# Optimization experiments

Hardware: AMD Instinct MI355X
Metric: run time of the kernel (lower is better)

Reference implementation:

```python
import jax, jax.numpy as jnp
import numpy as np

B, S, E, H = 2, 2048, 1024, 16
DH = E // H  # 64
EPS = 1e-5


def layer_norm(x, g, b):
    mu = jnp.mean(x, axis=-1, keepdims=True)
    var = jnp.mean(jnp.square(x - mu), axis=-1, keepdims=True)
    return (x - mu) * jax.lax.rsqrt(var + EPS) * g + b


def setup_inputs() -> dict:
    key = jax.random.key(0)
    ks = jax.random.split(key, 12)
    s = lambda fan_in: 1.0 / np.sqrt(fan_in)
    return {
        "x": jax.random.normal(ks[0], (B, S, E), dtype=jnp.float32),
        "ln1_g": jnp.ones((E,), jnp.float32),
        "ln1_b": jnp.zeros((E,), jnp.float32),
        # per-head projections, batched over head axis: [H, E, DH]
        "Wq": jax.random.uniform(ks[1], (H, E, DH), jnp.float32, -s(E), s(E)),
        "Wk": jax.random.uniform(ks[2], (H, E, DH), jnp.float32, -s(E), s(E)),
        "Wv": jax.random.uniform(ks[3], (H, E, DH), jnp.float32, -s(E), s(E)),
        "Wo": jax.random.uniform(ks[4], (H * DH, E), jnp.float32, -s(H * DH), s(H * DH)),
        "bo": jax.random.uniform(ks[5], (E,), jnp.float32, -s(H * DH), s(H * DH)),
        "ln2_g": jnp.ones((E,), jnp.float32),
        "ln2_b": jnp.zeros((E,), jnp.float32),
        "W1": jax.random.uniform(ks[6], (E, 4 * E), jnp.float32, -s(E), s(E)),
        "b1": jax.random.uniform(ks[7], (4 * E,), jnp.float32, -s(E), s(E)),
        "W2": jax.random.uniform(ks[8], (4 * E, E), jnp.float32, -s(4 * E), s(4 * E)),
        "b2": jax.random.uniform(ks[9], (E,), jnp.float32, -s(4 * E), s(4 * E)),
    }


def reference(x, ln1_g, ln1_b, Wq, Wk, Wv, Wo, bo, ln2_g, ln2_b, W1, b1, W2, b2):
    b, s, e = x.shape
    # --- multi-head attention (pre-LN) ---
    h = layer_norm(x, ln1_g, ln1_b)
    q = jnp.einsum("bse,hed->bhsd", h, Wq)
    k = jnp.einsum("bse,hed->bhsd", h, Wk)
    v = jnp.einsum("bse,hed->bhsd", h, Wv)
    # NOTE: original scales by channel**-0.5 (embed_size), not head_size
    scores = jnp.einsum("bhsd,bhtd->bhst", q, k) * (e ** -0.5)
    causal = jnp.tril(jnp.ones((s, s), dtype=bool))
    scores = jnp.where(causal, scores, -jnp.inf)
    attn = jax.nn.softmax(scores, axis=-1)  # dropout is identity in eval
    out = jnp.einsum("bhst,bhtd->bhsd", attn, v)
    out = out.transpose(0, 2, 1, 3).reshape(b, s, -1)  # concat heads: [B,S,H*DH]
    x = x + out @ Wo + bo
    # --- feed-forward (pre-LN) ---
    h2 = layer_norm(x, ln2_g, ln2_b)
    ff = jax.nn.relu(h2 @ W1 + b1) @ W2 + b2
    return x + ff
```

## Files before the change

kernel.cpp:

```cpp
#include <hip/hip_runtime.h>


typedef __bf16 bf16_t;
typedef __attribute__((ext_vector_type(8))) __bf16 bf16x8;
typedef __attribute__((ext_vector_type(4))) __bf16 bf16x4;
typedef __attribute__((ext_vector_type(4))) float f32x4;

#define B_DIM 2
#define S_DIM 2048
#define E_DIM 1024
#define H_DIM 16
#define DH_DIM 64

#define GLD16(gp, lp) __builtin_amdgcn_global_load_lds( \
    (const __attribute__((address_space(1))) void*)(gp), \
    (__attribute__((address_space(3))) void*)(lp), 16, 0, 0)

#define Q_SCALE 0.0450842120f

__global__ __launch_bounds__(256) void ln_kernel(
    const float* __restrict__ x, const float* __restrict__ g,
    const float* __restrict__ bv, bf16_t* __restrict__ out)
{
  const int row = blockIdx.x;
  const int t = threadIdx.x;
  const float* xr = x + (size_t)row * E_DIM;
  float4 v = *(const float4*)&xr[t * 4];
  float s  = v.x + v.y + v.z + v.w;
  float s2 = v.x*v.x + v.y*v.y + v.z*v.z + v.w*v.w;
#pragma unroll
  for (int m = 1; m < 64; m <<= 1) {
    s  += __shfl_xor(s,  m, 64);
    s2 += __shfl_xor(s2, m, 64);
  }
  __shared__ float red[8];
  const int wid = t >> 6, lane = t & 63;
  if (lane == 0) { red[wid] = s; red[4 + wid] = s2; }
  __syncthreads();
  s  = red[0] + red[1] + red[2] + red[3];
  s2 = red[4] + red[5] + red[6] + red[7];
  const float mu  = s * (1.f / E_DIM);
  const float var = s2 * (1.f / E_DIM) - mu * mu;
  const float rs  = rsqrtf(var + 1e-5f);
  float4 gg = *(const float4*)&g[t * 4];
  float4 bb = *(const float4*)&bv[t * 4];
  bf16x4 o;
  o[0] = (bf16_t)((v.x - mu) * rs * gg.x + bb.x);
  o[1] = (bf16_t)((v.y - mu) * rs * gg.y + bb.y);
  o[2] = (bf16_t)((v.z - mu) * rs * gg.z + bb.z);
  o[3] = (bf16_t)((v.w - mu) * rs * gg.w + bb.w);
  *(bf16x4*)&out[(size_t)row * E_DIM + t * 4] = o;
}

__global__ __launch_bounds__(256) void reduce2_ln(
    const float* __restrict__ p, const float* __restrict__ bo,
    const float* __restrict__ x, const float* __restrict__ g,
    const float* __restrict__ bv, float* __restrict__ xmid, bf16_t* __restrict__ h2)
{
  const int row = blockIdx.x;
  const int t = threadIdx.x;
  const size_t off = (size_t)row * E_DIM + t * 4;
  float4 a  = *(const float4*)&p[off];
  float4 b4 = *(const float4*)&p[(size_t)4096 * E_DIM + off];
  float4 xr = *(const float4*)&x[off];
  float4 bo4 = *(const float4*)&bo[t * 4];
  float4 v;
  v.x = a.x + b4.x + xr.x + bo4.x;
  v.y = a.y + b4.y + xr.y + bo4.y;
  v.z = a.z + b4.z + xr.z + bo4.z;
  v.w = a.w + b4.w + xr.w + bo4.w;
  *(float4*)&xmid[off] = v;
  float s  = v.x + v.y + v.z + v.w;
  float s2 = v.x*v.x + v.y*v.y + v.z*v.z + v.w*v.w;
#pragma unroll
  for (int m = 1; m < 64; m <<= 1) {
    s  += __shfl_xor(s,  m, 64);
    s2 += __shfl_xor(s2, m, 64);
  }
  __shared__ float red[8];
  const int wid = t >> 6, lane = t & 63;
  if (lane == 0) { red[wid] = s; red[4 + wid] = s2; }
  __syncthreads();
  s  = red[0] + red[1] + red[2] + red[3];
  s2 = red[4] + red[5] + red[6] + red[7];
  const float mu  = s * (1.f / E_DIM);
  const float var = s2 * (1.f / E_DIM) - mu * mu;
  const float rs  = rsqrtf(var + 1e-5f);
  float4 gg = *(const float4*)&g[t * 4];
  float4 bb = *(const float4*)&bv[t * 4];
  bf16x4 o;
  o[0] = (bf16_t)((v.x - mu) * rs * gg.x + bb.x);
  o[1] = (bf16_t)((v.y - mu) * rs * gg.y + bb.y);
  o[2] = (bf16_t)((v.z - mu) * rs * gg.z + bb.z);
  o[3] = (bf16_t)((v.w - mu) * rs * gg.w + bb.w);
  *(bf16x4*)&h2[off] = o;
}

__global__ __launch_bounds__(256) void reduce4(
    const bf16_t* __restrict__ p0, const bf16_t* __restrict__ p1,
    const bf16_t* __restrict__ p2, const bf16_t* __restrict__ p3,
    const float* __restrict__ b2, const float* __restrict__ xm,
    float* __restrict__ out)
{
  const int row = blockIdx.x;
  const int t = threadIdx.x;
  const size_t off = (size_t)row * E_DIM + t * 4;
  bf16x4 a0 = *(const bf16x4*)&p0[off];
  bf16x4 a1 = *(const bf16x4*)&p1[off];
  bf16x4 a2 = *(const bf16x4*)&p2[off];
  bf16x4 a3 = *(const bf16x4*)&p3[off];
  float4 xr = *(const float4*)&xm[off];
  float4 bb = *(const float4*)&b2[t * 4];
  float4 o;
  o.x = (float)a0[0] + (float)a1[0] + (float)a2[0] + (float)a3[0] + xr.x + bb.x;
  o.y = (float)a0[1] + (float)a1[1] + (float)a2[1] + (float)a3[1] + xr.y + bb.y;
  o.z = (float)a0[2] + (float)a1[2] + (float)a2[2] + (float)a3[2] + xr.z + bb.z;
  o.w = (float)a0[3] + (float)a1[3] + (float)a2[3] + (float)a3[3] + xr.w + bb.w;
  *(float4*)&out[off] = o;
}

__global__ __launch_bounds__(256) void transpose_cast(
    const float* __restrict__ src, bf16_t* __restrict__ dst, int R, int C)
{
  __shared__ float tile[64][65];
  const int c0 = blockIdx.x * 64, r0 = blockIdx.y * 64;
  const int t = threadIdx.x;
  const int rr = t >> 2;
#pragma unroll
  for (int u = 0; u < 4; u++) {
    const int cc = (t & 3) * 4 + u * 16;
    float4 f = *(const float4*)&src[(size_t)(r0 + rr) * C + c0 + cc];
    tile[rr][cc + 0] = f.x; tile[rr][cc + 1] = f.y;
    tile[rr][cc + 2] = f.z; tile[rr][cc + 3] = f.w;
  }
  __syncthreads();
  const int oc = t >> 2;
#pragma unroll
  for (int u = 0; u < 4; u++) {
    const int orr = (t & 3) * 4 + u * 16;
    bf16x4 w;
    w[0] = (bf16_t)tile[orr + 0][oc];
    w[1] = (bf16_t)tile[orr + 1][oc];
    w[2] = (bf16_t)tile[orr + 2][oc];
    w[3] = (bf16_t)tile[orr + 3][oc];
    *(bf16x4*)&dst[(size_t)(c0 + oc) * R + r0 + orr] = w;
  }
}

__global__ __launch_bounds__(256) void qkv_transpose(
    const float* __restrict__ Wq, const float* __restrict__ Wk,
    const float* __restrict__ Wv, bf16_t* __restrict__ dstT)
{
  const int m = blockIdx.y >> 4, h = blockIdx.y & 15;
  const float* src = (m == 0 ? Wq : (m == 1 ? Wk : Wv)) + (size_t)h * E_DIM * DH_DIM;
  const int e0 = blockIdx.x * 64;
  __shared__ float tile[64][65];
  const int t = threadIdx.x;
  const int rr = t >> 2;
#pragma unroll
  for (int u = 0; u < 4; u++) {
    const int cc = (t & 3) * 4 + u * 16;
    float4 f = *(const float4*)&src[(size_t)(e0 + rr) * DH_DIM + cc];
    tile[rr][cc + 0] = f.x; tile[rr][cc + 1] = f.y;
    tile[rr][cc + 2] = f.z; tile[rr][cc + 3] = f.w;
  }
  __syncthreads();
  const int oc = t >> 2;
  const size_t drow = (size_t)(m * 1024 + h * 64 + oc) * E_DIM;
#pragma unroll
  for (int u = 0; u < 4; u++) {
    const int orr = (t & 3) * 4 + u * 16;
    bf16x4 w;
    w[0] = (bf16_t)tile[orr + 0][oc];
    w[1] = (bf16_t)tile[orr + 1][oc];
    w[2] = (bf16_t)tile[orr + 2][oc];
    w[3] = (bf16_t)tile[orr + 3][oc];
    *(bf16x4*)&dstT[drow + e0 + orr] = w;
  }
}

constexpr int EPI_QKV = 0, EPI_BIAS_RELU = 2, EPI_PART_F32 = 3, EPI_PART_B16 = 4;

template <int EPI>
__global__ __launch_bounds__(256) void gemm_kernel(
    const bf16_t* __restrict__ A, const bf16_t* __restrict__ Bt,
    int M, int N, int Kst, int Klen,
    const float* __restrict__ bias, const float* __restrict__ resid,
    float* __restrict__ outF, bf16_t* __restrict__ outB,
    bf16_t* __restrict__ qo, bf16_t* __restrict__ ko, bf16_t* __restrict__ vo)
{
  __shared__ bf16_t As[2][128 * 32];
  __shared__ bf16_t Bs[2][128 * 32];
  const int gx = gridDim.x;
  const int nwg = gx * gridDim.y;
  int id = blockIdx.y * gx + blockIdx.x;
  id = (id & 7) * (nwg >> 3) + (id >> 3);
  const int m0 = (id % gx) * 128, n0 = (id / gx) * 128;
  const int sp = blockIdx.z;
  A  += (size_t)sp * Klen;
  Bt += (size_t)sp * Klen;

  const int tid = threadIdx.x, lane = tid & 63, wid = tid >> 6;
  const int wr = wid >> 1, wc = wid & 1;
  const int lr = lane & 15, lg = lane >> 4;
  const int rl = lane >> 2, k8 = (lane & 3) * 8;

  auto stage = [&](int buf, int k0) {
#pragma unroll
    for (int q = 0; q < 2; q++) {
      const int row = q * 64 + wid * 16 + rl;
      GLD16(A  + (size_t)(m0 + row) * Kst + k0 + k8, &As[buf][(q * 64 + wid * 16) * 32]);
      GLD16(Bt + (size_t)(n0 + row) * Kst + k0 + k8, &Bs[buf][(q * 64 + wid * 16) * 32]);
    }
  };

  const f32x4 z4 = {0.f, 0.f, 0.f, 0.f};
  f32x4 acc[4][4];
#pragma unroll
  for (int i = 0; i < 4; i++)
#pragma unroll
    for (int j = 0; j < 4; j++) acc[i][j] = z4;

  const int nt = Klen / 32;
  stage(0, 0);
  for (int it = 0; it < nt; ++it) {
    const int cur = it & 1;
    __syncthreads();
    if (it + 1 < nt) stage(cur ^ 1, (it + 1) * 32);
    bf16x8 af[4], bfr[4];
#pragma unroll
    for (int i = 0; i < 4; i++)
      af[i]  = *(const bf16x8*)&As[cur][(wr * 64 + i * 16 + lr) * 32 + lg * 8];
#pragma unroll
    for (int j = 0; j < 4; j++)
      bfr[j] = *(const bf16x8*)&Bs[cur][(wc * 64 + j * 16 + lr) * 32 + lg * 8];
    __builtin_amdgcn_s_setprio(1);
#pragma unroll
    for (int i = 0; i < 4; i++)
#pragma unroll
      for (int j = 0; j < 4; j++)
        acc[i][j] = __builtin_amdgcn_mfma_f32_16x16x32_bf16(af[i], bfr[j], acc[i][j], 0, 0, 0);
    __builtin_amdgcn_s_setprio(0);
  }

#pragma unroll
  for (int i = 0; i < 4; i++) {
#pragma unroll
    for (int j = 0; j < 4; j++) {
#pragma unroll
      for (int r = 0; r < 4; r++) {
        const int m = m0 + wr * 64 + i * 16 + lg * 4 + r;
        const int n = n0 + wc * 64 + j * 16 + lr;
        const float val = acc[i][j][r];
        if constexpr (EPI == EPI_QKV) {
          const int tsel = n >> 10, h = (n >> 6) & 15, d = n & 63;
          const int b = m >> 11, s = m & 2047;
          const size_t idx = ((size_t)((b * H_DIM + h) * S_DIM + s)) * DH_DIM + d;
          if (tsel == 0)      qo[idx] = (bf16_t)(val * Q_SCALE);
          else if (tsel == 1) ko[idx] = (bf16_t)val;
          else                vo[idx] = (bf16_t)val;
        } else if constexpr (EPI == EPI_BIAS_RELU) {
          const float u = val + bias[n];
          outB[(size_t)m * N + n] = (bf16_t)(u > 0.f ? u : 0.f);
        } else if constexpr (EPI == EPI_PART_F32) {
          outF[(size_t)sp * M * N + (size_t)m * N + n] = val;
        } else {
          bf16_t* o = sp == 0 ? outB : sp == 1 ? qo : sp == 2 ? ko : vo;
          o[(size_t)m * N + n] = (bf16_t)val;
        }
      }
    }
  }
}

__global__ __launch_bounds__(256) void attn_kernel(
    const bf16_t* __restrict__ Q, const bf16_t* __restrict__ K,
    const bf16_t* __restrict__ V, bf16_t* __restrict__ O,
    bf16_t* __restrict__ Opart, float* __restrict__ mpart, float* __restrict__ lpart)
{
  __shared__ bf16_t Ks[2][64 * 64];
  __shared__ bf16_t Vst[2][64 * 64];
  __shared__ bf16_t Ps[4][16 * 64];

  const int nwg = 80 * gridDim.y;
  int id = blockIdx.y * 80 + blockIdx.x;
  id = (id & 7) * (nwg >> 3) + (id >> 3);
  const int bx = id % 80, bh = id / 80;

  int qt, sp, ns;
  if (bx < 8)       { qt = bx;                sp = 0;            ns = 1; }
  else if (bx < 24) { qt = 8 + ((bx - 8) >> 1);  sp = (bx - 8) & 1;  ns = 2; }
  else if (bx < 48) { const int u = bx - 24; const int q3 = u / 3;
                      qt = 16 + q3;           sp = u - q3 * 3;   ns = 3; }
  else              { const int u = bx - 48;  qt = 24 + (u >> 2); sp = u & 3; ns = 4; }
  const int n = qt + 1;
  const int lo = (sp * n) / ns, hi = ((sp + 1) * n) / ns;

  const int q0b = qt * 64;
  const int tid = threadIdx.x;
  const int wid = tid >> 6, lane = tid & 63;
  const int lr = lane & 15, lg = lane >> 4;
  const int q0w = q0b + wid * 16;

  const bf16_t* Qp = Q + (size_t)bh * S_DIM * DH_DIM;
  const bf16_t* Kp = K + (size_t)bh * S_DIM * DH_DIM;
  const bf16_t* Vp = V + (size_t)bh * S_DIM * DH_DIM;

  bf16x8 bq[2];
#pragma unroll
  for (int c = 0; c < 2; c++)
    bq[c] = *(const bf16x8*)&Qp[(size_t)(q0w + lr) * DH_DIM + c * 32 + lg * 8];

  const f32x4 z4 = {0.f, 0.f, 0.f, 0.f};
  f32x4 Ot[4];
#pragma unroll
  for (int dt = 0; dt < 4; dt++) Ot[dt] = z4;
  float mrow = -1e30f, lrow = 0.f;

  const int st = tid >> 3;
  const int s8 = tid & 7;
  const int sbl = lane & 48;
  const int ktr = wid * 8 + (lane >> 3);
  const int ksc = (lane & 7);

  {
    const int t0 = lo * 64;
#pragma unroll
    for (int p = 0; p < 2; p++) {
      const int tr = p * 32 + ktr;
      GLD16(Kp + (size_t)(t0 + tr) * DH_DIM + (ksc ^ (tr & 7)) * 8,
            &Ks[0][(p * 32 + wid * 8) * 64]);
    }
  }
  bf16x8 vc0 = *(const bf16x8*)&Vp[(size_t)(lo * 64 + st) * DH_DIM + s8 * 8];
  bf16x8 vc1 = *(const bf16x8*)&Vp[(size_t)(lo * 64 + 32 + st) * DH_DIM + s8 * 8];
  bf16x8 vn0 = vc0, vn1 = vc1;

  for (int tc = lo; tc < hi; ++tc) {
    const int cur = (tc - lo) & 1;
#pragma unroll
    for (int h2 = 0; h2 < 2; h2++) {
      const bf16x8 vv = h2 ? vc1 : vc0;
      const int t = h2 * 32 + st;
#pragma unroll
      for (int j = 0; j < 8; j++) {
        const int d = s8 * 8 + j;
        const int f = j ^ s8;
        Vst[cur][(d * 128 + ((t * 2) ^ (f << 4))) >> 1] = vv[j];
      }
    }
    __syncthreads();
    if (tc + 1 < hi) {
      const int t1 = (tc + 1) * 64;
#pragma unroll
      for (int p = 0; p < 2; p++) {
        const int tr = p * 32 + ktr;
        GLD16(Kp + (size_t)(t1 + tr) * DH_DIM + (ksc ^ (tr & 7)) * 8,
              &Ks[cur ^ 1][(p * 32 + wid * 8) * 64]);
      }
      vn0 = *(const bf16x8*)&Vp[(size_t)(t1 + st) * DH_DIM + s8 * 8];
      vn1 = *(const bf16x8*)&Vp[(size_t)(t1 + 32 + st) * DH_DIM + s8 * 8];
    }

    const int t0 = tc * 64;
    f32x4 sc[4];
    __builtin_amdgcn_s_setprio(1);
#pragma unroll
    for (int j = 0; j < 4; j++) {
      f32x4 s = z4;
      const int t = j * 16 + lr;
#pragma unroll
      for (int c = 0; c < 2; c++) {
        const int kbyte = t * 128 + (((c * 4 + lg) * 16) ^ ((t & 7) << 4));
        bf16x8 ak = *(const bf16x8*)((const char*)&Ks[cur][0] + kbyte);
        s = __builtin_amdgcn_mfma_f32_16x16x32_bf16(ak, bq[c], s, 0, 0, 0);
      }
      sc[j] = s;
    }
    __builtin_amdgcn_s_setprio(0);
    if (tc == qt) {
#pragma unroll
      for (int j = 0; j < 4; j++)
#pragma unroll
        for (int r = 0; r < 4; r++) {
          const int tg = t0 + j * 16 + lg * 4 + r;
          if (tg > q0w + lr) sc[j][r] = -1e30f;
        }
    }
    float tmax = sc[0][0];
#pragma unroll
    for (int j = 0; j < 4; j++)
#pragma unroll
      for (int r = 0; r < 4; r++) tmax = fmaxf(tmax, sc[j][r]);
    tmax = fmaxf(tmax, __shfl_xor(tmax, 16, 64));
    tmax = fmaxf(tmax, __shfl_xor(tmax, 32, 64));
    const float mnew = fmaxf(mrow, tmax);
    const float fsc = __builtin_exp2f(mrow - mnew);
    mrow = mnew;
    float tsum = 0.f;
#pragma unroll
    for (int j = 0; j < 4; j++)
#pragma unroll
      for (int r = 0; r < 4; r++) {
        const float p = __builtin_exp2f(sc[j][r] - mnew);
        sc[j][r] = p;
        tsum += p;
      }
    tsum += __shfl_xor(tsum, 16, 64);
    tsum += __shfl_xor(tsum, 32, 64);
    lrow = lrow * fsc + tsum;

#pragma unroll
    for (int j = 0; j < 4; j++) {
      bf16x4 w;
#pragma unroll
      for (int r = 0; r < 4; r++) w[r] = (bf16_t)sc[j][r];
      const int pbyte = lr * 128 + ((j * 32 + lg * 8) ^ ((lr & 7) << 4));
      *(bf16x4*)((char*)&Ps[wid][0] + pbyte) = w;
    }
    float fr[4];
#pragma unroll
    for (int r = 0; r < 4; r++) fr[r] = __shfl(fsc, sbl | (lg * 4 + r), 64);
#pragma unroll
    for (int dt = 0; dt < 4; dt++)
#pragma unroll
      for (int r = 0; r < 4; r++) Ot[dt][r] *= fr[r];
    __builtin_amdgcn_s_setprio(1);
#pragma unroll
    for (int c = 0; c < 2; c++) {
      const int abyte = lr * 128 + ((c * 64 + lg * 16) ^ ((lr & 7) << 4));
      bf16x8 pa = *(const bf16x8*)((const char*)&Ps[wid][0] + abyte);
#pragma unroll
      for (int dt = 0; dt < 4; dt++) {
        const int d = dt * 16 + lr;
        const int f = (d & 7) ^ ((d >> 3) & 7);
        const int vbyte = d * 128 + (((c * 4 + lg) * 16) ^ (f << 4));
        bf16x8 bv = *(const bf16x8*)((const char*)&Vst[cur][0] + vbyte);
        Ot[dt] = __builtin_amdgcn_mfma_f32_16x16x32_bf16(pa, bv, Ot[dt], 0, 0, 0);
      }
    }
    __builtin_amdgcn_s_setprio(0);
    vc0 = vn0; vc1 = vn1;
  }

  if (ns == 1) {
    float linv[4];
#pragma unroll
    for (int r = 0; r < 4; r++)
      linv[r] = 1.f / __shfl(lrow, sbl | (lg * 4 + r), 64);
    const int b = bh >> 4, h = bh & 15;
#pragma unroll
    for (int r = 0; r < 4; r++) {
      const int s = q0w + lg * 4 + r;
      const size_t base = ((size_t)(b * S_DIM + s)) * E_DIM + h * DH_DIM;
#pragma unroll
      for (int dt = 0; dt < 4; dt++)
        O[base + dt * 16 + lr] = (bf16_t)(Ot[dt][r] * linv[r]);
    }
  } else {
    const int sbase = (qt < 16) ? 8 + 2 * (qt - 8)
                     : (qt < 24) ? 24 + 3 * (qt - 16) : 48 + 4 * (qt - 24);
    const int slot = bh * 80 + sbase + sp;
    bf16_t* Ob = Opart + (size_t)slot * 64 * 64;
#pragma unroll
    for (int r = 0; r < 4; r++)
#pragma unroll
      for (int dt = 0; dt < 4; dt++)
        Ob[(wid * 16 + lg * 4 + r) * 64 + dt * 16 + lr] = (bf16_t)Ot[dt][r];
    if (lg == 0) {
      mpart[slot * 64 + wid * 16 + lr] = mrow;
      lpart[slot * 64 + wid * 16 + lr] = lrow;
    }
  }
}

__global__ __launch_bounds__(256) void attn_combine(
    const bf16_t* __restrict__ Opart, const float* __restrict__ mpart,
    const float* __restrict__ lpart, bf16_t* __restrict__ O)
{
  const int qt = 8 + blockIdx.x;
  const int bh = blockIdx.y;
  const int ns = (qt < 16) ? 2 : (qt < 24) ? 3 : 4;
  const int sbase = (qt < 16) ? 8 + 2 * (qt - 8)
                   : (qt < 24) ? 24 + 3 * (qt - 16) : 48 + 4 * (qt - 24);
  const int slot0 = bh * 80 + sbase;
  const int tid = threadIdx.x;
  const int q = tid >> 2, d0 = (tid & 3) * 16;

  float M = -1e30f;
  for (int s = 0; s < ns; s++) M = fmaxf(M, mpart[(slot0 + s) * 64 + q]);
  float L = 0.f;
  float acc[16];
#pragma unroll
  for (int j = 0; j < 16; j++) acc[j] = 0.f;
  for (int s = 0; s < ns; s++) {
    const float w = __builtin_exp2f(mpart[(slot0 + s) * 64 + q] - M);
    L += w * lpart[(slot0 + s) * 64 + q];
    const bf16_t* Ob = Opart + ((size_t)(slot0 + s) * 64 + q) * 64 + d0;
    bf16x8 o0 = *(const bf16x8*)Ob;
    bf16x8 o1 = *(const bf16x8*)(Ob + 8);
#pragma unroll
    for (int j = 0; j < 8; j++) { acc[j] += w * (float)o0[j]; acc[8 + j] += w * (float)o1[j]; }
  }
  const float inv = 1.f / L;
  const int b = bh >> 4, h = bh & 15;
  const int srow = qt * 64 + q;
  bf16_t* out = O + ((size_t)(b * S_DIM + srow)) * E_DIM + h * DH_DIM + d0;
  bf16x8 w0, w1;
#pragma unroll
  for (int j = 0; j < 8; j++) { w0[j] = (bf16_t)(acc[j] * inv); w1[j] = (bf16_t)(acc[8 + j] * inv); }
  *(bf16x8*)out = w0;
  *(bf16x8*)(out + 8) = w1;
}

extern "C" void kernel_launch(void* const* d_in, const int* in_sizes, int n_in,
                              void* d_out, int out_size, void* d_ws, size_t ws_size,
                              hipStream_t stream)
{
  const float* x    = (const float*)d_in[0];
  const float* ln1g = (const float*)d_in[1];
  const float* ln1b = (const float*)d_in[2];
  const float* Wq   = (const float*)d_in[3];
  const float* Wk   = (const float*)d_in[4];
  const float* Wv   = (const float*)d_in[5];
  const float* Wo   = (const float*)d_in[6];
  const float* bo   = (const float*)d_in[7];
  const float* ln2g = (const float*)d_in[8];
  const float* ln2b = (const float*)d_in[9];
  const float* W1   = (const float*)d_in[10];
  const float* b1   = (const float*)d_in[11];
  const float* W2   = (const float*)d_in[12];
  const float* b2   = (const float*)d_in[13];

  char* ws = (char*)d_ws;
  bf16_t* WqkvT = (bf16_t*)(ws + 0);
  bf16_t* WoT   = (bf16_t*)(ws + 6291456);
  bf16_t* W1T   = (bf16_t*)(ws + 8388608);
  bf16_t* W2T   = (bf16_t*)(ws + 16777216);
  bf16_t* h1    = (bf16_t*)(ws + 25165824);
  bf16_t* qb    = (bf16_t*)(ws + 33554432);
  bf16_t* kb    = (bf16_t*)(ws + 41943040);
  bf16_t* vb    = (bf16_t*)(ws + 50331648);
  bf16_t* attnb = (bf16_t*)(ws + 58720256);
  float*  xmid  = (float* )(ws + 67108864);
  bf16_t* h2    = (bf16_t*)(ws + 83886080);
  bf16_t* ff1   = (bf16_t*)(ws + 25165824);
  bf16_t* Opart = (bf16_t*)(ws + 67108864);
  float*  mpart = (float* )(ws + 25165824);
  float*  lpart = (float* )(ws + 25821184);
  float*  po    = (float* )(ws + 25165824);
  bf16_t* pf0   = (bf16_t*)(ws + 0);
  bf16_t* pf1   = (bf16_t*)(ws + 8388608);
  bf16_t* pf2   = (bf16_t*)(ws + 58720256);
  bf16_t* pf3   = (bf16_t*)(ws + 83886080);

  qkv_transpose<<<dim3(16, 48), 256, 0, stream>>>(Wq, Wk, Wv, WqkvT);
  transpose_cast<<<dim3(16, 16), 256, 0, stream>>>(Wo, WoT, 1024, 1024);
  transpose_cast<<<dim3(64, 16), 256, 0, stream>>>(W1, W1T, 1024, 4096);
  transpose_cast<<<dim3(16, 64), 256, 0, stream>>>(W2, W2T, 4096, 1024);

  ln_kernel<<<4096, 256, 0, stream>>>(x, ln1g, ln1b, h1);
  gemm_kernel<EPI_QKV><<<dim3(32, 24, 1), 256, 0, stream>>>(
      h1, WqkvT, 4096, 3072, 1024, 1024, nullptr, nullptr,
      nullptr, nullptr, qb, kb, vb);
  attn_kernel<<<dim3(80, 32), 256, 0, stream>>>(qb, kb, vb, attnb, Opart, mpart, lpart);
  attn_combine<<<dim3(24, 32), 256, 0, stream>>>(Opart, mpart, lpart, attnb);
  gemm_kernel<EPI_PART_F32><<<dim3(32, 8, 2), 256, 0, stream>>>(
      attnb, WoT, 4096, 1024, 1024, 512, nullptr, nullptr,
      po, nullptr, nullptr, nullptr, nullptr);
  reduce2_ln<<<4096, 256, 0, stream>>>(po, bo, x, ln2g, ln2b, xmid, h2);
  gemm_kernel<EPI_BIAS_RELU><<<dim3(32, 32, 1), 256, 0, stream>>>(
      h2, W1T, 4096, 4096, 1024, 1024, b1, nullptr,
      nullptr, ff1, nullptr, nullptr, nullptr);
  gemm_kernel<EPI_PART_B16><<<dim3(32, 8, 4), 256, 0, stream>>>(
      ff1, W2T, 4096, 1024, 4096, 1024, nullptr, nullptr,
      nullptr, pf0, pf1, pf2, pf3);
  reduce4<<<4096, 256, 0, stream>>>(pf0, pf1, pf2, pf3, b2, xmid, (float*)d_out);

  (void)in_sizes; (void)n_in; (void)out_size; (void)ws_size;
}
```

Measured before the change: 284.9 us.

## Use 256x256 GEMM tiles with 512 threads, triple-buffered LDS and XOR swizzle

Replaces the 128x128, 256-thread GEMM with a 256x256 tile computed by 8 waves, each owning 128x64 of the output. LDS staging moves to a three-buffer ring with explicit vmcnt waits and raw barriers, so two tiles are in flight, and an XOR swizzle of the k-chunk is meant to reduce LDS bank conflicts. The aim is more data reuse per loaded byte and better latency hiding. The cost is fewer workgroups: the Wo GEMM gets only 128 blocks and the W2 GEMM 256, which can leave CUs idle on a 256-CU part. Register pressure also rises with 128 accumulator floats per thread.

```diff
diff --git a/kernel.cpp b/kernel.cpp
--- a/kernel.cpp
+++ b/kernel.cpp
@@ -182,80 +182,97 @@
 constexpr int EPI_QKV = 0, EPI_BIAS_RELU = 2, EPI_PART_F32 = 3, EPI_PART_B16 = 4;
 
 template <int EPI>
-__global__ __launch_bounds__(256) void gemm_kernel(
+__global__ __launch_bounds__(512, 2) void gemm256_kernel(
     const bf16_t* __restrict__ A, const bf16_t* __restrict__ Bt,
     int M, int N, int Kst, int Klen,
-    const float* __restrict__ bias, const float* __restrict__ resid,
+    const float* __restrict__ bias,
     float* __restrict__ outF, bf16_t* __restrict__ outB,
     bf16_t* __restrict__ qo, bf16_t* __restrict__ ko, bf16_t* __restrict__ vo)
 {
-  __shared__ bf16_t As[2][128 * 32];
-  __shared__ bf16_t Bs[2][128 * 32];
+  __shared__ bf16_t As[3][256 * 32];
+  __shared__ bf16_t Bs[3][256 * 32];
+
   const int gx = gridDim.x;
   const int nwg = gx * gridDim.y;
   int id = blockIdx.y * gx + blockIdx.x;
   id = (id & 7) * (nwg >> 3) + (id >> 3);
-  const int m0 = (id % gx) * 128, n0 = (id / gx) * 128;
+  const int m0 = (id % gx) * 256, n0 = (id / gx) * 256;
   const int sp = blockIdx.z;
   A  += (size_t)sp * Klen;
   Bt += (size_t)sp * Klen;
 
   const int tid = threadIdx.x, lane = tid & 63, wid = tid >> 6;
-  const int wr = wid >> 1, wc = wid & 1;
+  const int wm = wid >> 2, wn = wid & 3;
   const int lr = lane & 15, lg = lane >> 4;
-  const int rl = lane >> 2, k8 = (lane & 3) * 8;
-
-  auto stage = [&](int buf, int k0) {
-#pragma unroll
-    for (int q = 0; q < 2; q++) {
-      const int row = q * 64 + wid * 16 + rl;
-      GLD16(A  + (size_t)(m0 + row) * Kst + k0 + k8, &As[buf][(q * 64 + wid * 16) * 32]);
-      GLD16(Bt + (size_t)(n0 + row) * Kst + k0 + k8, &Bs[buf][(q * 64 + wid * 16) * 32]);
+
+  auto stage = [&](int kt, int buf) {
+#pragma unroll
+    for (int p = 0; p < 2; p++) {
+      const int s = p * 512 + tid;
+      const int r = s >> 2;
+      const int sl = (s & 3) ^ (r & 3);
+      const int ldsoff = (p * 512 + wid * 64) * 8;
+      GLD16(A  + (size_t)(m0 + r) * Kst + kt * 32 + sl * 8, &As[buf][ldsoff]);
+      GLD16(Bt + (size_t)(n0 + r) * Kst + kt * 32 + sl * 8, &Bs[buf][ldsoff]);
     }
   };
 
   const f32x4 z4 = {0.f, 0.f, 0.f, 0.f};
-  f32x4 acc[4][4];
-#pragma unroll
-  for (int i = 0; i < 4; i++)
+  f32x4 acc[8][4];
+#pragma unroll
+  for (int i = 0; i < 8; i++)
 #pragma unroll
     for (int j = 0; j < 4; j++) acc[i][j] = z4;
 
-  const int nt = Klen / 32;
+  const int NT = Klen / 32;
   stage(0, 0);
-  for (int it = 0; it < nt; ++it) {
-    const int cur = it & 1;
-    __syncthreads();
-    if (it + 1 < nt) stage(cur ^ 1, (it + 1) * 32);
-    bf16x8 af[4], bfr[4];
-#pragma unroll
-    for (int i = 0; i < 4; i++)
-      af[i]  = *(const bf16x8*)&As[cur][(wr * 64 + i * 16 + lr) * 32 + lg * 8];
-#pragma unroll
-    for (int j = 0; j < 4; j++)
-      bfr[j] = *(const bf16x8*)&Bs[cur][(wc * 64 + j * 16 + lr) * 32 + lg * 8];
+  stage(1, 1);
+  for (int T = 0; T < NT; ++T) {
+    const int b = T % 3;
+    if (T + 2 < NT) {
+      asm volatile("s_waitcnt vmcnt(4)" ::: "memory");
+      __builtin_amdgcn_s_barrier();
+      stage(T + 2, (T + 2) % 3);
+    } else if (T + 1 < NT) {
+      asm volatile("s_waitcnt vmcnt(4)" ::: "memory");
+      __builtin_amdgcn_s_barrier();
+    } else {
+      asm volatile("s_waitcnt vmcnt(0)" ::: "memory");
+      __builtin_amdgcn_s_barrier();
+    }
+    __builtin_amdgcn_sched_barrier(0);
+
+    bf16x8 bfr[4];
+#pragma unroll
+    for (int j = 0; j < 4; j++) {
+      const int r = wn * 64 + j * 16 + lr;
+      bfr[j] = *(const bf16x8*)&Bs[b][r * 32 + ((lg ^ (lr & 3)) * 8)];
+    }
     __builtin_amdgcn_s_setprio(1);
 #pragma unroll
-    for (int i = 0; i < 4; i++)
+    for (int i = 0; i < 8; i++) {
+      const int r = wm * 128 + i * 16 + lr;
+      bf16x8 af = *(const bf16x8*)&As[b][r * 32 + ((lg ^ (lr & 3)) * 8)];
 #pragma unroll
       for (int j = 0; j < 4; j++)
-        acc[i][j] = __builtin_amdgcn_mfma_f32_16x16x32_bf16(af[i], bfr[j], acc[i][j], 0, 0, 0);
+        acc[i][j] = __builtin_amdgcn_mfma_f32_16x16x32_bf16(af, bfr[j], acc[i][j], 0, 0, 0);
+    }
     __builtin_amdgcn_s_setprio(0);
   }
 
 #pragma unroll
-  for (int i = 0; i < 4; i++) {
+  for (int i = 0; i < 8; i++) {
 #pragma unroll
     for (int j = 0; j < 4; j++) {
 #pragma unroll
       for (int r = 0; r < 4; r++) {
-        const int m = m0 + wr * 64 + i * 16 + lg * 4 + r;
-        const int n = n0 + wc * 64 + j * 16 + lr;
+        const int m = m0 + wm * 128 + i * 16 + lg * 4 + r;
+        const int n = n0 + wn * 64 + j * 16 + lr;
         const float val = acc[i][j][r];
         if constexpr (EPI == EPI_QKV) {
           const int tsel = n >> 10, h = (n >> 6) & 15, d = n & 63;
-          const int b = m >> 11, s = m & 2047;
-          const size_t idx = ((size_t)((b * H_DIM + h) * S_DIM + s)) * DH_DIM + d;
+          const int b_ = m >> 11, s_ = m & 2047;
+          const size_t idx = ((size_t)((b_ * H_DIM + h) * S_DIM + s_)) * DH_DIM + d;
           if (tsel == 0)      qo[idx] = (bf16_t)(val * Q_SCALE);
           else if (tsel == 1) ko[idx] = (bf16_t)val;
           else                vo[idx] = (bf16_t)val;
@@ -560,20 +577,20 @@
   transpose_cast<<<dim3(16, 64), 256, 0, stream>>>(W2, W2T, 4096, 1024);
 
   ln_kernel<<<4096, 256, 0, stream>>>(x, ln1g, ln1b, h1);
-  gemm_kernel<EPI_QKV><<<dim3(32, 24, 1), 256, 0, stream>>>(
-      h1, WqkvT, 4096, 3072, 1024, 1024, nullptr, nullptr,
+  gemm256_kernel<EPI_QKV><<<dim3(16, 12, 1), 512, 0, stream>>>(
+      h1, WqkvT, 4096, 3072, 1024, 1024, nullptr,
       nullptr, nullptr, qb, kb, vb);
   attn_kernel<<<dim3(80, 32), 256, 0, stream>>>(qb, kb, vb, attnb, Opart, mpart, lpart);
   attn_combine<<<dim3(24, 32), 256, 0, stream>>>(Opart, mpart, lpart, attnb);
-  gemm_kernel<EPI_PART_F32><<<dim3(32, 8, 2), 256, 0, stream>>>(
-      attnb, WoT, 4096, 1024, 1024, 512, nullptr, nullptr,
+  gemm256_kernel<EPI_PART_F32><<<dim3(16, 4, 2), 512, 0, stream>>>(
+      attnb, WoT, 4096, 1024, 1024, 512, nullptr,
       po, nullptr, nullptr, nullptr, nullptr);
   reduce2_ln<<<4096, 256, 0, stream>>>(po, bo, x, ln2g, ln2b, xmid, h2);
-  gemm_kernel<EPI_BIAS_RELU><<<dim3(32, 32, 1), 256, 0, stream>>>(
-      h2, W1T, 4096, 4096, 1024, 1024, b1, nullptr,
+  gemm256_kernel<EPI_BIAS_RELU><<<dim3(16, 16, 1), 512, 0, stream>>>(
+      h2, W1T, 4096, 4096, 1024, 1024, b1,
       nullptr, ff1, nullptr, nullptr, nullptr);
-  gemm_kernel<EPI_PART_B16><<<dim3(32, 8, 4), 256, 0, stream>>>(
-      ff1, W2T, 4096, 1024, 4096, 1024, nullptr, nullptr,
+  gemm256_kernel<EPI_PART_B16><<<dim3(16, 4, 4), 512, 0, stream>>>(
+      ff1, W2T, 4096, 1024, 4096, 1024, nullptr,
       nullptr, pf0, pf1, pf2, pf3);
   reduce4<<<4096, 256, 0, stream>>>(pf0, pf1, pf2, pf3, b2, xmid, (float*)d_out);
 
```

Measured after the change: 289.6 us. About the same (+1.6%).
